# Kernel tuning notes

Hardware: AMD Instinct MI355X
Metric: run time of the kernel (lower is better)

Reference implementation:

```python
import jax, jax.numpy as jnp
import numpy as np


def setup_inputs() -> dict:
    key = jax.random.key(0)
    # [L, B, N, N] stacked list of batched dense adjacency matrices
    adj = jax.random.uniform(key, (2, 8, 2048, 2048), dtype=jnp.float32)
    return {"adj": adj}


def reference(adj):
    # degree = row-sum over last dim; inv-degree with NaN/Inf -> 0
    degree = jnp.sum(adj, axis=-1)                      # [L, B, N]
    inv = 1.0 / degree
    inv = jnp.where(jnp.isfinite(inv), inv, jnp.zeros_like(inv))
    # diag_embed(inv) @ adj == row-wise scale by inv
    normed = inv[..., None] * adj                       # [L, B, N, N]
    return normed
```

## Files before the change

kernel.cpp:

```cpp
#include <hip/hip_runtime.h>
#include <math.h>


#define ROW_N 2048
#define BLOCK 256

__global__ __launch_bounds__(BLOCK) void normalizer_kernel(
    const float* __restrict__ adj, float* __restrict__ out) {
  const size_t row = blockIdx.x;
  const float4* __restrict__ src =
      reinterpret_cast<const float4*>(adj + row * (size_t)ROW_N);
  float4* __restrict__ dst = reinterpret_cast<float4*>(out + row * (size_t)ROW_N);

  const int t = threadIdx.x;

  float4 v0 = src[t];
  float4 v1 = src[t + BLOCK];

  float local = (v0.x + v0.y) + (v0.z + v0.w) + (v1.x + v1.y) + (v1.z + v1.w);

  #pragma unroll
  for (int off = 32; off > 0; off >>= 1)
    local += __shfl_down(local, off, 64);

  __shared__ float wave_sums[BLOCK / 64];
  __shared__ float s_inv;
  if ((t & 63) == 0) wave_sums[t >> 6] = local;
  __syncthreads();

  if (t == 0) {
    float deg = (wave_sums[0] + wave_sums[1]) + (wave_sums[2] + wave_sums[3]);
    float inv = 1.0f / deg;
    if (!isfinite(inv)) inv = 0.0f;
    s_inv = inv;
  }
  __syncthreads();

  const float inv = s_inv;
  v0.x *= inv; v0.y *= inv; v0.z *= inv; v0.w *= inv;
  v1.x *= inv; v1.y *= inv; v1.z *= inv; v1.w *= inv;

  dst[t] = v0;
  dst[t + BLOCK] = v1;
}

extern "C" void kernel_launch(void* const* d_in, const int* in_sizes, int n_in,
                              void* d_out, int out_size, void* d_ws, size_t ws_size,
                              hipStream_t stream) {
  const float* adj = (const float*)d_in[0];
  float* out = (float*)d_out;
  const int rows = out_size / ROW_N;
  normalizer_kernel<<<rows, BLOCK, 0, stream>>>(adj, out);
}
```

Before: 424.9 us.

## Assign one wavefront per row to remove block-level LDS reduction and barriers

Each 64-lane wavefront now owns one full 2048-float row, loading 8 float4 per lane and reducing with xor shuffles so every lane holds the row sum. This drops the shared-memory partial sums and the two __syncthreads barriers, and a block now covers four rows. It raises per-thread register use (32 floats held) and cuts the block count by four, which may reduce memory-level parallelism per wave even as more loads are in flight per lane.

```diff
diff --git a/kernel.cpp b/kernel.cpp
--- a/kernel.cpp
+++ b/kernel.cpp
@@ -4,44 +4,44 @@
 
 #define ROW_N 2048
 #define BLOCK 256
+#define WAVES_PER_BLOCK (BLOCK / 64)
+#define F4_PER_LANE 8
 
 __global__ __launch_bounds__(BLOCK) void normalizer_kernel(
-    const float* __restrict__ adj, float* __restrict__ out) {
-  const size_t row = blockIdx.x;
+    const float* __restrict__ adj, float* __restrict__ out, int rows) {
+  const int wave = threadIdx.x >> 6;
+  const int lane = threadIdx.x & 63;
+  const int row = blockIdx.x * WAVES_PER_BLOCK + wave;
+  if (row >= rows) return;
+
   const float4* __restrict__ src =
-      reinterpret_cast<const float4*>(adj + row * (size_t)ROW_N);
-  float4* __restrict__ dst = reinterpret_cast<float4*>(out + row * (size_t)ROW_N);
+      reinterpret_cast<const float4*>(adj + (size_t)row * ROW_N);
+  float4* __restrict__ dst =
+      reinterpret_cast<float4*>(out + (size_t)row * ROW_N);
 
-  const int t = threadIdx.x;
+  float4 v[F4_PER_LANE];
+  #pragma unroll
+  for (int k = 0; k < F4_PER_LANE; ++k)
+    v[k] = src[lane + 64 * k];
 
-  float4 v0 = src[t];
-  float4 v1 = src[t + BLOCK];
-
-  float local = (v0.x + v0.y) + (v0.z + v0.w) + (v1.x + v1.y) + (v1.z + v1.w);
+  float local = 0.0f;
+  #pragma unroll
+  for (int k = 0; k < F4_PER_LANE; ++k)
+    local += (v[k].x + v[k].y) + (v[k].z + v[k].w);
 
   #pragma unroll
   for (int off = 32; off > 0; off >>= 1)
-    local += __shfl_down(local, off, 64);
+    local += __shfl_xor(local, off, 64);
 
-  __shared__ float wave_sums[BLOCK / 64];
-  __shared__ float s_inv;
-  if ((t & 63) == 0) wave_sums[t >> 6] = local;
-  __syncthreads();
+  float inv = 1.0f / local;
+  if (!isfinite(inv)) inv = 0.0f;
 
-  if (t == 0) {
-    float deg = (wave_sums[0] + wave_sums[1]) + (wave_sums[2] + wave_sums[3]);
-    float inv = 1.0f / deg;
-    if (!isfinite(inv)) inv = 0.0f;
-    s_inv = inv;
+  #pragma unroll
+  for (int k = 0; k < F4_PER_LANE; ++k) {
+    float4 r = v[k];
+    r.x *= inv; r.y *= inv; r.z *= inv; r.w *= inv;
+    dst[lane + 64 * k] = r;
   }
-  __syncthreads();
-
-  const float inv = s_inv;
-  v0.x *= inv; v0.y *= inv; v0.z *= inv; v0.w *= inv;
-  v1.x *= inv; v1.y *= inv; v1.z *= inv; v1.w *= inv;
-
-  dst[t] = v0;
-  dst[t + BLOCK] = v1;
 }
 
 extern "C" void kernel_launch(void* const* d_in, const int* in_sizes, int n_in,
@@ -50,5 +50,6 @@
   const float* adj = (const float*)d_in[0];
   float* out = (float*)d_out;
   const int rows = out_size / ROW_N;
-  normalizer_kernel<<<rows, BLOCK, 0, stream>>>(adj, out);
+  const int grid = (rows + WAVES_PER_BLOCK - 1) / WAVES_PER_BLOCK;
+  normalizer_kernel<<<grid, BLOCK, 0, stream>>>(adj, out, rows);
 }
```

New measurement: 432.1 us. Within noise of the previous version (+1.7%).
